# Optimization experiments

Measured on AMD Instinct MI355X. Metric: run time of the kernel, lower is better.

Reference implementation:

```python
import jax, jax.numpy as jnp
import numpy as np

C = 512
GROUPS = 8
EPS = 1e-5


def setup_inputs() -> dict:
    key = jax.random.key(0)
    ks = jax.random.split(key, 7)
    B, H, W = 16, 32, 32
    x = jax.random.normal(ks[0], (B, C, H, W), dtype=jnp.float32)
    gn_w = jnp.ones((C,), jnp.float32)
    gn_b = jnp.zeros((C,), jnp.float32)
    s = 1.0 / np.sqrt(C)
    qkv_w = jax.random.normal(ks[1], (3 * C, C), dtype=jnp.float32) * s
    qkv_b = jnp.zeros((3 * C,), jnp.float32)
    proj_w = jax.random.normal(ks[2], (C, C), dtype=jnp.float32) * s
    proj_b = jnp.zeros((C,), jnp.float32)
    return {"x": x, "gn_w": gn_w, "gn_b": gn_b, "qkv_w": qkv_w,
            "qkv_b": qkv_b, "proj_w": proj_w, "proj_b": proj_b}


def _group_norm(x, w, b):
    B, Cc, H, W = x.shape
    xg = x.reshape(B, GROUPS, Cc // GROUPS, H, W)
    mean = xg.mean(axis=(2, 3, 4), keepdims=True)
    var = xg.var(axis=(2, 3, 4), keepdims=True)
    xn = ((xg - mean) * jax.lax.rsqrt(var + EPS)).reshape(B, Cc, H, W)
    return xn * w[None, :, None, None] + b[None, :, None, None]


def reference(x, gn_w, gn_b, qkv_w, qkv_b, proj_w, proj_b):
    B, Cc, H, W = x.shape
    N = H * W
    h = _group_norm(x, gn_w, gn_b)
    # 1x1 conv == per-pixel matmul over channels
    qkv = jnp.einsum('bchw,oc->bohw', h, qkv_w) + qkv_b[None, :, None, None]
    q, k, v = jnp.split(qkv, 3, axis=1)          # each (B, C, H, W)
    q = q.reshape(B, Cc, N).transpose(0, 2, 1)   # (B, N, C)
    k = k.reshape(B, Cc, N)                      # (B, C, N)
    v = v.reshape(B, Cc, N).transpose(0, 2, 1)   # (B, N, C)
    attn = jnp.einsum('bnc,bcm->bnm', q, k) * (Cc ** -0.5)
    attn = jax.nn.softmax(attn, axis=-1)
    h = jnp.einsum('bnm,bmc->bnc', attn, v)      # (B, N, C)
    h = h.transpose(0, 2, 1).reshape(B, Cc, H, W)
    out = jnp.einsum('bchw,oc->bohw', h, proj_w) + proj_b[None, :, None, None]
    return x + out
```

## Files before the change

kernel.cpp:

```cpp
#include <hip/hip_runtime.h>


typedef __bf16 bf16x8 __attribute__((ext_vector_type(8)));
typedef float f32x4 __attribute__((ext_vector_type(4)));
typedef unsigned short u16x8 __attribute__((ext_vector_type(8)));
typedef unsigned short u16x4 __attribute__((ext_vector_type(4)));

#define DEVINL __device__ __forceinline__

DEVINL float b2f(unsigned short u) {
  unsigned int x = ((unsigned int)u) << 16;
  return __builtin_bit_cast(float, x);
}
DEVINL unsigned short f2b(float f) {
  unsigned int x = __builtin_bit_cast(unsigned int, f);
  x += 0x7fffu + ((x >> 16) & 1u);
  return (unsigned short)(x >> 16);
}

DEVINL void gload16(const void* g, void* l) {
  __builtin_amdgcn_global_load_lds(
      (const __attribute__((address_space(1))) unsigned int*)(const void*)g,
      (__attribute__((address_space(3))) unsigned int*)l, 16, 0, 0);
}

__global__ __launch_bounds__(256)
void f2bf_k(const float* __restrict__ in, unsigned short* __restrict__ out, int n4) {
  int i = blockIdx.x * 256 + threadIdx.x;
  if (i < n4) {
    float4 v = ((const float4*)in)[i];
    u16x4 o;
    o[0] = f2b(v.x); o[1] = f2b(v.y); o[2] = f2b(v.z); o[3] = f2b(v.w);
    ((u16x4*)out)[i] = o;
  }
}

__global__ __launch_bounds__(256)
void gn_stats(const float* __restrict__ x, float* __restrict__ mean, float* __restrict__ rstd) {
  const int g = blockIdx.x;
  const float4* p = (const float4*)(x + (long long)g * 65536);
  float s = 0.f, q = 0.f;
  for (int i = threadIdx.x; i < 16384; i += 256) {
    float4 v = p[i];
    s += v.x + v.y + v.z + v.w;
    q += v.x * v.x + v.y * v.y + v.z * v.z + v.w * v.w;
  }
#pragma unroll
  for (int off = 32; off; off >>= 1) { s += __shfl_xor(s, off); q += __shfl_xor(q, off); }
  __shared__ float ss[4], qs[4];
  const int wave = threadIdx.x >> 6, lane = threadIdx.x & 63;
  if (lane == 0) { ss[wave] = s; qs[wave] = q; }
  __syncthreads();
  if (threadIdx.x == 0) {
    float S = ss[0] + ss[1] + ss[2] + ss[3];
    float Q = qs[0] + qs[1] + qs[2] + qs[3];
    float mu = S * (1.f / 65536.f);
    float var = Q * (1.f / 65536.f) - mu * mu;
    mean[g] = mu;
    rstd[g] = rsqrtf(var + 1e-5f);
  }
}

__global__ __launch_bounds__(256)
void gn_apply_t(const float* __restrict__ x, const float* __restrict__ mean,
                const float* __restrict__ rstd, const float* __restrict__ gw,
                const float* __restrict__ gb, unsigned short* __restrict__ h) {
  const int b = blockIdx.z, ct = blockIdx.y, pt = blockIdx.x;
  const int c0 = ct << 6, p0 = pt << 6;
  const float mu = mean[b * 8 + ct];
  const float rs = rstd[b * 8 + ct];
  __shared__ float t[64][65];
  const int r4 = threadIdx.x >> 6, cl = threadIdx.x & 63;
#pragma unroll
  for (int i = 0; i < 16; ++i) {
    int r = i * 4 + r4;
    int c = c0 + r;
    float v = x[(long long)(b * 512 + c) * 1024 + p0 + cl];
    t[r][cl] = (v - mu) * rs * gw[c] + gb[c];
  }
  __syncthreads();
#pragma unroll
  for (int i = 0; i < 16; ++i) {
    int pr = i * 4 + r4;
    h[(long long)(b * 1024 + p0 + pr) * 512 + c0 + cl] = f2b(t[cl][pr]);
  }
}

__global__ __launch_bounds__(256)
void vtrans(const unsigned short* __restrict__ qkv, unsigned short* __restrict__ vt) {
  const int b = blockIdx.z, ct = blockIdx.y, pt = blockIdx.x;
  const int c0 = ct << 6, p0 = pt << 6;
  const unsigned short* src = qkv + (long long)b * 1024 * 1536 + 1024;
  unsigned short* dst = vt + (long long)b * 512 * 1024;
  __shared__ unsigned short t[64][65];
  const int r4 = threadIdx.x >> 6, cl = threadIdx.x & 63;
#pragma unroll
  for (int i = 0; i < 16; ++i) {
    int pr = i * 4 + r4;
    t[pr][cl] = src[(long long)(p0 + pr) * 1536 + c0 + cl];
  }
  __syncthreads();
#pragma unroll
  for (int i = 0; i < 16; ++i) {
    int cr = i * 4 + r4;
    dst[(long long)(c0 + cr) * 1024 + p0 + cl] = t[cl][cr];
  }
}

__global__ __launch_bounds__(256)
void softmax_rows(unsigned short* __restrict__ S) {
  const long long row = (long long)blockIdx.x * 4 + (threadIdx.x >> 6);
  const int lane = threadIdx.x & 63;
  u16x8* p = (u16x8*)(S + row * 1024);
  u16x8 a = p[lane], b = p[64 + lane];
  float v[16];
#pragma unroll
  for (int i = 0; i < 8; ++i) { v[i] = b2f(a[i]); v[8 + i] = b2f(b[i]); }
  float m = v[0];
#pragma unroll
  for (int i = 1; i < 16; ++i) m = fmaxf(m, v[i]);
#pragma unroll
  for (int off = 32; off; off >>= 1) m = fmaxf(m, __shfl_xor(m, off));
  float s = 0.f;
#pragma unroll
  for (int i = 0; i < 16; ++i) { v[i] = __expf(v[i] - m); s += v[i]; }
#pragma unroll
  for (int off = 32; off; off >>= 1) s += __shfl_xor(s, off);
  float inv = 1.f / s;
#pragma unroll
  for (int i = 0; i < 8; ++i) { a[i] = f2b(v[i] * inv); b[i] = f2b(v[8 + i] * inv); }
  p[lane] = a;
  p[64 + lane] = b;
}

#define RSQRT_C 0.044194173824159216f
enum { EPI_BF16 = 0, EPI_QKV = 1, EPI_PROJ = 2 };

template <int EPI>
__global__ __launch_bounds__(256)
void gemm_bt(const unsigned short* __restrict__ A, int lda, long long sA,
             const unsigned short* __restrict__ B, int ldb, long long sB,
             void* __restrict__ Cv, int ldc, long long sC, int K,
             const float* __restrict__ bias, const float* __restrict__ resid) {
  __shared__ char lds[32768];
  const int tid = threadIdx.x;
  const int wave = tid >> 6, lane = tid & 63;
  const int wr = wave >> 1, wc = wave & 1;
  const long long bm = blockIdx.y, bn = blockIdx.x, bz = blockIdx.z;

  const unsigned short* Ab = A + bz * sA + bm * 128 * (long long)lda;
  const unsigned short* Bb = B + bz * sB + bn * 128 * (long long)ldb;

  f32x4 acc[4][4] = {};

  const int frow = lane & 15;
  const int fk = (lane >> 4) << 3;

  for (int k0 = 0; k0 < K; k0 += 64) {
#pragma unroll
    for (int i = 0; i < 4; ++i) {
      int chunk = (i << 8) + tid;
      int r = chunk >> 3, c8 = chunk & 7;
      const unsigned short* ga = Ab + (long long)r * lda + k0 + (c8 << 3);
      const unsigned short* gb = Bb + (long long)r * ldb + k0 + (c8 << 3);
      char* la = lds + (((i << 8) + (wave << 6)) << 4);
      gload16(ga, la);
      gload16(gb, la + 16384);
    }
    __syncthreads();
#pragma unroll
    for (int ks = 0; ks < 2; ++ks) {
      bf16x8 af[4], bfr[4];
#pragma unroll
      for (int f = 0; f < 4; ++f) {
        int ar = (wr << 6) + (f << 4) + frow;
        af[f] = *reinterpret_cast<const bf16x8*>(lds + ((ar << 6) + (ks << 5) + fk) * 2);
        int br = (wc << 6) + (f << 4) + frow;
        bfr[f] = *reinterpret_cast<const bf16x8*>(lds + 16384 + ((br << 6) + (ks << 5) + fk) * 2);
      }
#pragma unroll
      for (int i = 0; i < 4; ++i)
#pragma unroll
        for (int j = 0; j < 4; ++j)
          acc[i][j] = __builtin_amdgcn_mfma_f32_16x16x32_bf16(af[i], bfr[j], acc[i][j], 0, 0, 0);
    }
    __syncthreads();
  }

  const int rb = (int)bm * 128 + (wr << 6) + ((lane >> 4) << 2);
  const int cb = (int)bn * 128 + (wc << 6) + (lane & 15);
#pragma unroll
  for (int i = 0; i < 4; ++i) {
#pragma unroll
    for (int j = 0; j < 4; ++j) {
      const int col = cb + (j << 4);
#pragma unroll
      for (int r = 0; r < 4; ++r) {
        const int row = rb + (i << 4) + r;
        float v = acc[i][j][r];
        if constexpr (EPI == EPI_BF16) {
          ((unsigned short*)Cv)[bz * sC + (long long)row * ldc + col] = f2b(v);
        } else if constexpr (EPI == EPI_QKV) {
          v += bias[col];
          if (col < 512) v *= RSQRT_C;
          ((unsigned short*)Cv)[bz * sC + (long long)row * ldc + col] = f2b(v);
        } else {
          long long idx = bz * sC + (long long)row * ldc + col;
          ((float*)Cv)[idx] = v + bias[row] + resid[idx];
        }
      }
    }
  }
}

extern "C" void kernel_launch(void* const* d_in, const int* in_sizes, int n_in,
                              void* d_out, int out_size, void* d_ws, size_t ws_size,
                              hipStream_t stream) {
  const float* x      = (const float*)d_in[0];
  const float* gn_w   = (const float*)d_in[1];
  const float* gn_b   = (const float*)d_in[2];
  const float* qkv_w  = (const float*)d_in[3];
  const float* qkv_b  = (const float*)d_in[4];
  const float* proj_w = (const float*)d_in[5];
  const float* proj_b = (const float*)d_in[6];

  char* ws = (char*)d_ws;
  float* mean          = (float*)(ws + 0);
  float* rstd          = (float*)(ws + 512);
  unsigned short* wq   = (unsigned short*)(ws + 1024);
  unsigned short* wp   = (unsigned short*)(ws + 1573888);
  unsigned short* h    = (unsigned short*)(ws + 2098176);
  unsigned short* qkv  = (unsigned short*)(ws + 18875392);
  unsigned short* vt   = h;
  unsigned short* O    = qkv;
  unsigned short* S    = (unsigned short*)d_out;

  f2bf_k<<<768, 256, 0, stream>>>(qkv_w, wq, 196608);
  f2bf_k<<<256, 256, 0, stream>>>(proj_w, wp, 65536);
  gn_stats<<<128, 256, 0, stream>>>(x, mean, rstd);
  gn_apply_t<<<dim3(16, 8, 16), 256, 0, stream>>>(x, mean, rstd, gn_w, gn_b, h);
  gemm_bt<EPI_QKV><<<dim3(12, 128, 1), 256, 0, stream>>>(
      h, 512, 0, wq, 512, 0, qkv, 1536, 0, 512, qkv_b, nullptr);
  gemm_bt<EPI_BF16><<<dim3(8, 8, 16), 256, 0, stream>>>(
      qkv, 1536, 1024LL * 1536, qkv + 512, 1536, 1024LL * 1536,
      S, 1024, 1024LL * 1024, 512, nullptr, nullptr);
  softmax_rows<<<4096, 256, 0, stream>>>(S);
  vtrans<<<dim3(16, 8, 16), 256, 0, stream>>>(qkv, vt);
  gemm_bt<EPI_BF16><<<dim3(4, 8, 16), 256, 0, stream>>>(
      S, 1024, 1024LL * 1024, vt, 1024, 512LL * 1024,
      O, 512, 1024LL * 512, 1024, nullptr, nullptr);
  gemm_bt<EPI_PROJ><<<dim3(8, 4, 16), 256, 0, stream>>>(
      wp, 512, 0, O, 512, 1024LL * 512,
      d_out, 1024, 512LL * 1024, 512, proj_b, x);
}
```

Baseline: 280.8 us.

## Double-buffer GEMM LDS tiles with XOR swizzle and XCD-aware block remap

Rewrites the shared GEMM mainloop to prefetch two K-tiles into a double-buffered 64KB LDS. Global loads for tile k+2 are issued while tile k is computed, using vmcnt waits and raw barriers instead of __syncthreads. LDS columns are XOR-swizzled by row to reduce bank conflicts on the fragment reads. The grid is flattened to 1D and block IDs are remapped across the 8 XCDs to improve L2 locality. The larger LDS footprint limits occupancy, and the hand-counted waitcnt logic is easy to get wrong.

New measurement: 243.8 us. 1.15x faster.

```diff
diff --git a/kernel.cpp b/kernel.cpp
--- a/kernel.cpp
+++ b/kernel.cpp
@@ -136,47 +136,69 @@
 #define RSQRT_C 0.044194173824159216f
 enum { EPI_BF16 = 0, EPI_QKV = 1, EPI_PROJ = 2 };
 
+DEVINL void stage_tile(const unsigned short* __restrict__ Ab,
+                       const unsigned short* __restrict__ Bb,
+                       int lda, int ldb, int k0, char* lb, int tid, int wave) {
+#pragma unroll
+  for (int i = 0; i < 4; ++i) {
+    const int c = (i << 8) + tid;
+    const int r = c >> 3;
+    const int sk = ((c & 7) ^ (r & 7)) << 3;
+    char* la = lb + (((i << 8) + (wave << 6)) << 4);
+    gload16(Ab + (long long)r * lda + k0 + sk, la);
+    gload16(Bb + (long long)r * ldb + k0 + sk, la + 16384);
+  }
+}
+
 template <int EPI>
-__global__ __launch_bounds__(256)
+__global__ __launch_bounds__(256, 2)
 void gemm_bt(const unsigned short* __restrict__ A, int lda, long long sA,
              const unsigned short* __restrict__ B, int ldb, long long sB,
              void* __restrict__ Cv, int ldc, long long sC, int K,
-             const float* __restrict__ bias, const float* __restrict__ resid) {
-  __shared__ char lds[32768];
+             const float* __restrict__ bias, const float* __restrict__ resid,
+             int gx, int gy) {
+  __shared__ char lds[65536];
   const int tid = threadIdx.x;
   const int wave = tid >> 6, lane = tid & 63;
   const int wr = wave >> 1, wc = wave & 1;
-  const long long bm = blockIdx.y, bn = blockIdx.x, bz = blockIdx.z;
-
-  const unsigned short* Ab = A + bz * sA + bm * 128 * (long long)lda;
-  const unsigned short* Bb = B + bz * sB + bn * 128 * (long long)ldb;
+
+  const int nwg = gridDim.x;
+  const int id0 = blockIdx.x;
+  const int id = (id0 & 7) * (nwg >> 3) + (id0 >> 3);
+  const int bn = id % gx;
+  const int t1 = id / gx;
+  const int bm = t1 % gy;
+  const int bz = t1 / gy;
+
+  const unsigned short* Ab = A + (long long)bz * sA + (long long)bm * 128 * lda;
+  const unsigned short* Bb = B + (long long)bz * sB + (long long)bn * 128 * ldb;
 
   f32x4 acc[4][4] = {};
-
   const int frow = lane & 15;
-  const int fk = (lane >> 4) << 3;
-
-  for (int k0 = 0; k0 < K; k0 += 64) {
-#pragma unroll
-    for (int i = 0; i < 4; ++i) {
-      int chunk = (i << 8) + tid;
-      int r = chunk >> 3, c8 = chunk & 7;
-      const unsigned short* ga = Ab + (long long)r * lda + k0 + (c8 << 3);
-      const unsigned short* gb = Bb + (long long)r * ldb + k0 + (c8 << 3);
-      char* la = lds + (((i << 8) + (wave << 6)) << 4);
-      gload16(ga, la);
-      gload16(gb, la + 16384);
-    }
-    __syncthreads();
+  const int fkb = (lane >> 4) << 4;
+  const int swr = (frow & 7) << 4;
+  const int NT = K >> 6;
+
+  stage_tile(Ab, Bb, lda, ldb, 0, lds, tid, wave);
+  stage_tile(Ab, Bb, lda, ldb, 64, lds + 32768, tid, wave);
+  asm volatile("s_waitcnt vmcnt(8)" ::: "memory");
+
+  for (int kt = 0; kt < NT; ++kt) {
+    const int cur = kt & 1;
+    __builtin_amdgcn_s_barrier();
+    asm volatile("" ::: "memory");
+    const char* lb = lds + cur * 32768;
+    __builtin_amdgcn_s_setprio(1);
 #pragma unroll
     for (int ks = 0; ks < 2; ++ks) {
       bf16x8 af[4], bfr[4];
+      const int kb = (ks << 6) + fkb;
 #pragma unroll
       for (int f = 0; f < 4; ++f) {
-        int ar = (wr << 6) + (f << 4) + frow;
-        af[f] = *reinterpret_cast<const bf16x8*>(lds + ((ar << 6) + (ks << 5) + fk) * 2);
-        int br = (wc << 6) + (f << 4) + frow;
-        bfr[f] = *reinterpret_cast<const bf16x8*>(lds + 16384 + ((br << 6) + (ks << 5) + fk) * 2);
+        const int ar = (wr << 6) + (f << 4) + frow;
+        af[f] = *reinterpret_cast<const bf16x8*>(lb + ar * 128 + (kb ^ swr));
+        const int br = (wc << 6) + (f << 4) + frow;
+        bfr[f] = *reinterpret_cast<const bf16x8*>(lb + 16384 + br * 128 + (kb ^ swr));
       }
 #pragma unroll
       for (int i = 0; i < 4; ++i)
@@ -184,11 +206,19 @@
         for (int j = 0; j < 4; ++j)
           acc[i][j] = __builtin_amdgcn_mfma_f32_16x16x32_bf16(af[i], bfr[j], acc[i][j], 0, 0, 0);
     }
-    __syncthreads();
-  }
-
-  const int rb = (int)bm * 128 + (wr << 6) + ((lane >> 4) << 2);
-  const int cb = (int)bn * 128 + (wc << 6) + (lane & 15);
+    __builtin_amdgcn_s_setprio(0);
+    asm volatile("" ::: "memory");
+    __builtin_amdgcn_s_barrier();
+    if (kt + 2 < NT) {
+      stage_tile(Ab, Bb, lda, ldb, (kt + 2) << 6, lds + cur * 32768, tid, wave);
+      asm volatile("s_waitcnt vmcnt(8)" ::: "memory");
+    } else if (kt + 2 == NT) {
+      asm volatile("s_waitcnt vmcnt(0)" ::: "memory");
+    }
+  }
+
+  const int rb = bm * 128 + (wr << 6) + ((lane >> 4) << 2);
+  const int cb = bn * 128 + (wc << 6) + (lane & 15);
 #pragma unroll
   for (int i = 0; i < 4; ++i) {
 #pragma unroll
@@ -199,13 +229,13 @@
         const int row = rb + (i << 4) + r;
         float v = acc[i][j][r];
         if constexpr (EPI == EPI_BF16) {
-          ((unsigned short*)Cv)[bz * sC + (long long)row * ldc + col] = f2b(v);
+          ((unsigned short*)Cv)[(long long)bz * sC + (long long)row * ldc + col] = f2b(v);
         } else if constexpr (EPI == EPI_QKV) {
           v += bias[col];
           if (col < 512) v *= RSQRT_C;
-          ((unsigned short*)Cv)[bz * sC + (long long)row * ldc + col] = f2b(v);
+          ((unsigned short*)Cv)[(long long)bz * sC + (long long)row * ldc + col] = f2b(v);
         } else {
-          long long idx = bz * sC + (long long)row * ldc + col;
+          long long idx = (long long)bz * sC + (long long)row * ldc + col;
           ((float*)Cv)[idx] = v + bias[row] + resid[idx];
         }
       }
@@ -239,17 +269,17 @@
   f2bf_k<<<256, 256, 0, stream>>>(proj_w, wp, 65536);
   gn_stats<<<128, 256, 0, stream>>>(x, mean, rstd);
   gn_apply_t<<<dim3(16, 8, 16), 256, 0, stream>>>(x, mean, rstd, gn_w, gn_b, h);
-  gemm_bt<EPI_QKV><<<dim3(12, 128, 1), 256, 0, stream>>>(
-      h, 512, 0, wq, 512, 0, qkv, 1536, 0, 512, qkv_b, nullptr);
-  gemm_bt<EPI_BF16><<<dim3(8, 8, 16), 256, 0, stream>>>(
+  gemm_bt<EPI_QKV><<<1536, 256, 0, stream>>>(
+      h, 512, 0, wq, 512, 0, qkv, 1536, 0, 512, qkv_b, nullptr, 12, 128);
+  gemm_bt<EPI_BF16><<<1024, 256, 0, stream>>>(
       qkv, 1536, 1024LL * 1536, qkv + 512, 1536, 1024LL * 1536,
-      S, 1024, 1024LL * 1024, 512, nullptr, nullptr);
+      S, 1024, 1024LL * 1024, 512, nullptr, nullptr, 8, 8);
   softmax_rows<<<4096, 256, 0, stream>>>(S);
   vtrans<<<dim3(16, 8, 16), 256, 0, stream>>>(qkv, vt);
-  gemm_bt<EPI_BF16><<<dim3(4, 8, 16), 256, 0, stream>>>(
+  gemm_bt<EPI_BF16><<<512, 256, 0, stream>>>(
       S, 1024, 1024LL * 1024, vt, 1024, 512LL * 1024,
-      O, 512, 1024LL * 512, 1024, nullptr, nullptr);
-  gemm_bt<EPI_PROJ><<<dim3(8, 4, 16), 256, 0, stream>>>(
+      O, 512, 1024LL * 512, 1024, nullptr, nullptr, 4, 8);
+  gemm_bt<EPI_PROJ><<<512, 256, 0, stream>>>(
       wp, 512, 0, O, 512, 1024LL * 512,
-      d_out, 1024, 512LL * 1024, 512, proj_b, x);
-}
+      d_out, 1024, 512LL * 1024, 512, proj_b, x, 8, 4);
+}
```
